# Optimization experiments

Measured on AMD Instinct MI355X. Metric: run time of the kernel, lower is better.

## Reference

```python
import jax, jax.numpy as jnp
import numpy as np

T = 512           # num_timestamps
D = 512           # video_embed_dim
V = 2048          # fmri_dim (voxels)
H = 128           # hidden_dim


def setup_inputs() -> dict:
    key = jax.random.key(0)
    k = jax.random.split(key, 8)
    s1 = 1.0 / np.sqrt(D)
    s2 = 1.0 / np.sqrt(H)
    return {
        "video_embeddings": jax.random.normal(k[0], (T, D), dtype=jnp.float32),
        # stacked per-voxel weights (torch Linear: y = x @ W.T + b; we store W already transposed as [in, out])
        "W1": jax.random.uniform(k[1], (V, D, H), jnp.float32, -s1, s1),
        "b1": jax.random.uniform(k[2], (V, H), jnp.float32, -s1, s1),
        "W2": jax.random.uniform(k[3], (V, H, H), jnp.float32, -s2, s2),
        "b2": jax.random.uniform(k[4], (V, H), jnp.float32, -s2, s2),
        "W3": jax.random.uniform(k[5], (V, H), jnp.float32, -s2, s2),
        "b3": jax.random.uniform(k[6], (V,), jnp.float32, -s2, s2),
    }


def reference(video_embeddings, W1, b1, W2, b2, W3, b3):
    # Per-voxel MLP expressed as batched GEMMs over the voxel axis.
    # Dropout is identity in eval mode.
    h = jax.nn.relu(jnp.einsum("td,vdh->tvh", video_embeddings, W1) + b1)  # [T,V,H]
    h = jax.nn.relu(jnp.einsum("tvh,vhg->tvg", h, W2) + b2)                 # [T,V,H]
    out = jnp.einsum("tvh,vh->tv", h, W3) + b3                               # [T,V]
    return out
```

## Files before the change

kernel.cpp:

```cpp
#include <hip/hip_runtime.h>
#include <hip/hip_bf16.h>

#define TT 512
#define DD 512
#define VV 2048
#define HH 128

typedef __attribute__((ext_vector_type(8))) short bf16x8;
typedef __attribute__((ext_vector_type(8))) unsigned short ushort8;
typedef __attribute__((ext_vector_type(4))) unsigned short ushort4v;
typedef __attribute__((ext_vector_type(4))) float f32x4;

__device__ __forceinline__ unsigned short f2bf(float f) {
  union { __hip_bfloat16 b; unsigned short u; } cv;
  cv.b = __float2bfloat16(f);
  return cv.u;
}

__device__ __forceinline__ void lds_barrier() {
  asm volatile("s_waitcnt lgkmcnt(0)\n\ts_barrier" ::: "memory");
}

#define VM_GATE(N)                                                   \
  do {                                                               \
    asm volatile("s_waitcnt vmcnt(" #N ")" ::: "memory");            \
    __builtin_amdgcn_sched_barrier(0);                               \
  } while (0)

__global__ void cvt_x_kernel(const float* __restrict__ x, unsigned short* __restrict__ xb) {
  const int i = blockIdx.x * blockDim.x + threadIdx.x;
  const float4 f = ((const float4*)x)[i];
  ushort4v u;
  u[0] = f2bf(f.x); u[1] = f2bf(f.y); u[2] = f2bf(f.z); u[3] = f2bf(f.w);
  ((ushort4v*)xb)[i] = u;
}

__global__ __launch_bounds__(512, 2)
void voxel_mlp_kernel(const unsigned short* __restrict__ Xb,
                      const float* __restrict__ W1,
                      const float* __restrict__ b1,
                      const float* __restrict__ W2,
                      const float* __restrict__ b2,
                      const float* __restrict__ W3,
                      const float* __restrict__ b3,
                      float* __restrict__ out) {
  __shared__ __align__(16) char LDS[98304];
  constexpr unsigned GBASE  = 0;
  constexpr unsigned FBASE  = 65536;
  constexpr unsigned W2BASE = 0;
  constexpr unsigned H1BASE = 32768;

  const int v   = blockIdx.x;
  const int tid = threadIdx.x;
  const int w   = tid >> 6;
  const int l   = tid & 63;
  const int lg  = l >> 4;
  const int ll  = l & 15;

  const float* W1v = W1 + (size_t)v * DD * HH;
  const float* W2v = W2 + (size_t)v * HH * HH;

  const size_t gsrc_lane = (size_t)((w * 8 + (l >> 5)) * HH + (l & 31) * 4);

#define G_ISSUE(t)                                                         \
  { const float* gp = W1v + (size_t)(t) * 64 * HH + gsrc_lane;             \
    const unsigned ldst = GBASE + (unsigned)((t) & 1) * 32768u +           \
                          (unsigned)w * 4096u;                             \
    _Pragma("unroll") for (int p = 0; p < 4; ++p)                          \
      __builtin_amdgcn_global_load_lds(                                    \
        (const __attribute__((address_space(1))) void*)(gp + p * 2 * HH),  \
        (__attribute__((address_space(3))) void*)(&LDS[ldst + p * 1024u]), \
        16, 0, 0); }

  G_ISSUE(0);
  G_ISSUE(1);

  f32x4 acc1[4][8];
#pragma unroll
  for (int mi = 0; mi < 4; ++mi)
#pragma unroll
    for (int n = 0; n < 8; ++n) acc1[mi][n] = f32x4{0.f, 0.f, 0.f, 0.f};

#pragma unroll
  for (int s = 0; s < 8; ++s) {
    VM_GATE(4);
    lds_barrier();

    bf16x8 aF[2][4];
#pragma unroll
    for (int ks = 0; ks < 2; ++ks)
#pragma unroll
      for (int mi = 0; mi < 4; ++mi)
        aF[ks][mi] = *(const bf16x8*)(Xb + (size_t)(w * 64 + mi * 16 + ll) * DD +
                                      s * 64 + ks * 32 + lg * 8);

    const unsigned gb = GBASE + (unsigned)(s & 1) * 32768u;
#pragma unroll
    for (int ks = 0; ks < 2; ++ks) {
      float t0[8];
#pragma unroll
      for (int j = 0; j < 8; ++j)
        t0[j] = *(const float*)(&LDS[gb + (unsigned)(((ks * 32 + lg * 8 + j) * HH) +
                                                     w * 16 + ll) * 4u]);
      ushort8 e;
#pragma unroll
      for (int j = 0; j < 8; ++j) e[j] = f2bf(t0[j]);
      *(ushort8*)(&LDS[FBASE + (unsigned)ks * 8192u + (unsigned)w * 1024u +
                       (unsigned)l * 16u]) = e;
    }

    lds_barrier();

    if (s < 6) G_ISSUE(s + 2);

#pragma unroll
    for (int ks = 0; ks < 2; ++ks)
#pragma unroll
      for (int n = 0; n < 8; ++n) {
        const bf16x8 b = *(const bf16x8*)(&LDS[FBASE + (unsigned)ks * 8192u +
                                               (unsigned)n * 1024u + (unsigned)l * 16u]);
#pragma unroll
        for (int mi = 0; mi < 4; ++mi)
          acc1[mi][n] = __builtin_amdgcn_mfma_f32_16x16x32_bf16(aF[ks][mi], b, acc1[mi][n], 0, 0, 0);
      }
  }
#undef G_ISSUE


  float b1v[8], b2v[8], w3v[8];
#pragma unroll
  for (int n = 0; n < 8; ++n) {
    b1v[n] = b1[v * HH + n * 16 + ll];
    b2v[n] = b2[v * HH + n * 16 + ll];
    w3v[n] = W3[v * HH + n * 16 + ll];
  }
  const float b3v = b3[v];

  {
    const int ki = w & 3, mb = (w >> 2) * 4;
    float w2t[4][8];
#pragma unroll
    for (int q = 0; q < 4; ++q)
#pragma unroll
      for (int j = 0; j < 8; ++j)
        w2t[q][j] = W2v[(ki * 32 + lg * 8 + j) * HH + (mb + q) * 16 + ll];
#pragma unroll
    for (int q = 0; q < 4; ++q) {
      ushort8 e;
#pragma unroll
      for (int j = 0; j < 8; ++j) e[j] = f2bf(w2t[q][j]);
      *(ushort8*)(&LDS[W2BASE + (unsigned)ki * 8192u + (unsigned)(mb + q) * 1024u +
                       (unsigned)l * 16u]) = e;
    }
  }
  lds_barrier();

  const unsigned slot = H1BASE + (unsigned)w * 4096u;

#pragma unroll
  for (int mi = 0; mi < 4; ++mi) {
#pragma unroll
    for (int n = 0; n < 8; ++n) {
#pragma unroll
      for (int r = 0; r < 4; ++r) {
        const int tl = lg * 4 + r;
        float hv = acc1[mi][n][r] + b1v[n];
        hv = fmaxf(hv, 0.f);
        const int h = n * 16 + ll;
        const unsigned byte = slot + (unsigned)tl * 256u +
                              (unsigned)((h * 2) ^ ((tl & 7) << 4));
        *(unsigned short*)(&LDS[byte]) = f2bf(hv);
      }
    }
    f32x4 acc2[8];
#pragma unroll
    for (int m = 0; m < 8; ++m) acc2[m] = f32x4{0.f, 0.f, 0.f, 0.f};
#pragma unroll
    for (int ki = 0; ki < 4; ++ki) {
      const int k0 = ki * 32 + lg * 8;
      const unsigned abyte = slot + (unsigned)ll * 256u +
                             (unsigned)((k0 * 2) ^ ((ll & 7) << 4));
      const bf16x8 a2 = *(const bf16x8*)(&LDS[abyte]);
#pragma unroll
      for (int m = 0; m < 8; ++m) {
        const bf16x8 bw = *(const bf16x8*)(&LDS[W2BASE + (unsigned)ki * 8192u +
                                                (unsigned)m * 1024u + (unsigned)l * 16u]);
        acc2[m] = __builtin_amdgcn_mfma_f32_16x16x32_bf16(a2, bw, acc2[m], 0, 0, 0);
      }
    }
#pragma unroll
    for (int r = 0; r < 4; ++r) {
      float p = 0.f;
#pragma unroll
      for (int m = 0; m < 8; ++m)
        p += fmaxf(acc2[m][r] + b2v[m], 0.f) * w3v[m];
      p += __shfl_xor(p, 1);
      p += __shfl_xor(p, 2);
      p += __shfl_xor(p, 4);
      p += __shfl_xor(p, 8);
      if (ll == 0) {
        const int t = w * 64 + mi * 16 + lg * 4 + r;
        out[t * VV + v] = p + b3v;
      }
    }
  }
}

extern "C" void kernel_launch(void* const* d_in, const int* in_sizes, int n_in,
                              void* d_out, int out_size, void* d_ws, size_t ws_size,
                              hipStream_t stream) {
  const float* X  = (const float*)d_in[0];
  const float* W1 = (const float*)d_in[1];
  const float* b1 = (const float*)d_in[2];
  const float* W2 = (const float*)d_in[3];
  const float* b2 = (const float*)d_in[4];
  const float* W3 = (const float*)d_in[5];
  const float* b3 = (const float*)d_in[6];
  float* out = (float*)d_out;

  unsigned short* Xb = (unsigned short*)d_ws;

  cvt_x_kernel<<<256, 256, 0, stream>>>(X, Xb);
  voxel_mlp_kernel<<<VV, 512, 0, stream>>>(Xb, W1, b1, W2, b2, W3, b3, out);
}
```

Measured before the change: 298.1 us.

## Split each voxel across two blocks by time, triple-buffer W1 with smaller LDS

Launches two blocks per voxel, each handling half the timestamps, with an XCD-aware mapping so both halves of a voxel land on the same XCD and can share W1 reads through L2. LDS shrinks to 64KB and launch bounds rise so more blocks fit per CU. The W1 pipeline moves to 32-row steps with a three-slot fp32 staging ring, a swizzled bf16 fragment layout and a single barrier per step. In exchange each voxel's W1/W2 weights are fetched and converted twice, which doubles conversion work and risks extra HBM traffic if the L2 sharing does not happen.

```diff
diff --git a/kernel.cpp b/kernel.cpp
--- a/kernel.cpp
+++ b/kernel.cpp
@@ -35,7 +35,7 @@
   ((ushort4v*)xb)[i] = u;
 }
 
-__global__ __launch_bounds__(512, 2)
+__global__ __launch_bounds__(512, 4)
 void voxel_mlp_kernel(const unsigned short* __restrict__ Xb,
                       const float* __restrict__ W1,
                       const float* __restrict__ b1,
@@ -44,13 +44,18 @@
                       const float* __restrict__ W3,
                       const float* __restrict__ b3,
                       float* __restrict__ out) {
-  __shared__ __align__(16) char LDS[98304];
+  __shared__ __align__(16) char LDS[65536];
   constexpr unsigned GBASE  = 0;
-  constexpr unsigned FBASE  = 65536;
+  constexpr unsigned FBASE  = 49152;
   constexpr unsigned W2BASE = 0;
   constexpr unsigned H1BASE = 32768;
 
-  const int v   = blockIdx.x;
+  const int bid  = blockIdx.x;
+  const int xcd  = bid & 7;
+  const int gg   = bid >> 3;
+  const int half = gg & 1;
+  const int v    = (gg >> 1) * 8 + xcd;
+
   const int tid = threadIdx.x;
   const int w   = tid >> 6;
   const int l   = tid & 63;
@@ -60,72 +65,77 @@
   const float* W1v = W1 + (size_t)v * DD * HH;
   const float* W2v = W2 + (size_t)v * HH * HH;
 
-  const size_t gsrc_lane = (size_t)((w * 8 + (l >> 5)) * HH + (l & 31) * 4);
-
-#define G_ISSUE(t)                                                         \
-  { const float* gp = W1v + (size_t)(t) * 64 * HH + gsrc_lane;             \
-    const unsigned ldst = GBASE + (unsigned)((t) & 1) * 32768u +           \
-                          (unsigned)w * 4096u;                             \
-    _Pragma("unroll") for (int p = 0; p < 4; ++p)                          \
-      __builtin_amdgcn_global_load_lds(                                    \
-        (const __attribute__((address_space(1))) void*)(gp + p * 2 * HH),  \
-        (__attribute__((address_space(3))) void*)(&LDS[ldst + p * 1024u]), \
+  const size_t gsrc = (size_t)((w * 4 + (l >> 5)) * HH + (l & 31) * 4);
+  const int n_c = l >> 3;
+  const int ll0 = (l & 7) * 2;
+
+#define G_ISSUE(t)                                                          \
+  { const float* gp = W1v + (size_t)(t) * 32 * HH + gsrc;                   \
+    const unsigned ldst = GBASE + (unsigned)((t) % 3) * 16384u +            \
+                          (unsigned)w * 2048u;                              \
+    _Pragma("unroll") for (int p = 0; p < 2; ++p)                           \
+      __builtin_amdgcn_global_load_lds(                                     \
+        (const __attribute__((address_space(1))) void*)(gp + p * 2 * HH),   \
+        (__attribute__((address_space(3))) void*)(&LDS[ldst + p * 1024u]),  \
         16, 0, 0); }
+
+#define CVT(tau)                                                            \
+  { const unsigned gs = GBASE + (unsigned)((tau) % 3) * 16384u;             \
+    ushort4v ev, ov;                                                        \
+    _Pragma("unroll") for (int r = 0; r < 4; ++r) {                         \
+      const float2 g2 = *(const float2*)(&LDS[gs +                          \
+          (unsigned)((w * 4 + r) * 512 + (n_c * 16 + ll0) * 4)]);           \
+      ev[r] = f2bf(g2.x); ov[r] = f2bf(g2.y); }                             \
+    const unsigned fb = FBASE + (unsigned)((tau) & 1) * 8192u +             \
+                        (unsigned)n_c * 1024u;                              \
+    const unsigned ca = (unsigned)((((w >> 1) * 16 + ll0) * 16) ^ (n_c << 4)); \
+    const unsigned cb = (unsigned)((((w >> 1) * 16 + ll0 + 1) * 16) ^ (n_c << 4)); \
+    *(ushort4v*)(&LDS[fb + ca + (unsigned)(w & 1) * 8u]) = ev;              \
+    *(ushort4v*)(&LDS[fb + cb + (unsigned)(w & 1) * 8u]) = ov; }
 
   G_ISSUE(0);
   G_ISSUE(1);
-
-  f32x4 acc1[4][8];
-#pragma unroll
-  for (int mi = 0; mi < 4; ++mi)
+  VM_GATE(2);
+  CVT(0);
+  lds_barrier();
+
+  f32x4 acc1[2][8];
+#pragma unroll
+  for (int mi = 0; mi < 2; ++mi)
 #pragma unroll
     for (int n = 0; n < 8; ++n) acc1[mi][n] = f32x4{0.f, 0.f, 0.f, 0.f};
 
 #pragma unroll
-  for (int s = 0; s < 8; ++s) {
-    VM_GATE(4);
+  for (int s = 0; s < 16; ++s) {
+    bf16x8 aF[2];
+#pragma unroll
+    for (int mi = 0; mi < 2; ++mi)
+      aF[mi] = *(const bf16x8*)(Xb + (size_t)(half * 256 + w * 32 + mi * 16 + ll) * DD +
+                                s * 32 + lg * 8);
+    __builtin_amdgcn_sched_barrier(0);
+
+    if (s < 14) {
+      G_ISSUE(s + 2);
+      VM_GATE(2);
+    } else if (s == 14) {
+      VM_GATE(0);
+    }
+
+    if (s < 15) CVT(s + 1);
+
+#pragma unroll
+    for (int n = 0; n < 8; ++n) {
+      const bf16x8 b = *(const bf16x8*)(&LDS[FBASE + (unsigned)(s & 1) * 8192u +
+                                             (unsigned)n * 1024u +
+                                             (unsigned)(((lg * 16 + ll) * 16) ^ (n << 4))]);
+#pragma unroll
+      for (int mi = 0; mi < 2; ++mi)
+        acc1[mi][n] = __builtin_amdgcn_mfma_f32_16x16x32_bf16(aF[mi], b, acc1[mi][n], 0, 0, 0);
+    }
     lds_barrier();
-
-    bf16x8 aF[2][4];
-#pragma unroll
-    for (int ks = 0; ks < 2; ++ks)
-#pragma unroll
-      for (int mi = 0; mi < 4; ++mi)
-        aF[ks][mi] = *(const bf16x8*)(Xb + (size_t)(w * 64 + mi * 16 + ll) * DD +
-                                      s * 64 + ks * 32 + lg * 8);
-
-    const unsigned gb = GBASE + (unsigned)(s & 1) * 32768u;
-#pragma unroll
-    for (int ks = 0; ks < 2; ++ks) {
-      float t0[8];
-#pragma unroll
-      for (int j = 0; j < 8; ++j)
-        t0[j] = *(const float*)(&LDS[gb + (unsigned)(((ks * 32 + lg * 8 + j) * HH) +
-                                                     w * 16 + ll) * 4u]);
-      ushort8 e;
-#pragma unroll
-      for (int j = 0; j < 8; ++j) e[j] = f2bf(t0[j]);
-      *(ushort8*)(&LDS[FBASE + (unsigned)ks * 8192u + (unsigned)w * 1024u +
-                       (unsigned)l * 16u]) = e;
-    }
-
-    lds_barrier();
-
-    if (s < 6) G_ISSUE(s + 2);
-
-#pragma unroll
-    for (int ks = 0; ks < 2; ++ks)
-#pragma unroll
-      for (int n = 0; n < 8; ++n) {
-        const bf16x8 b = *(const bf16x8*)(&LDS[FBASE + (unsigned)ks * 8192u +
-                                               (unsigned)n * 1024u + (unsigned)l * 16u]);
-#pragma unroll
-        for (int mi = 0; mi < 4; ++mi)
-          acc1[mi][n] = __builtin_amdgcn_mfma_f32_16x16x32_bf16(aF[ks][mi], b, acc1[mi][n], 0, 0, 0);
-      }
   }
 #undef G_ISSUE
-
+#undef CVT
 
   float b1v[8], b2v[8], w3v[8];
 #pragma unroll
@@ -158,7 +168,7 @@
   const unsigned slot = H1BASE + (unsigned)w * 4096u;
 
 #pragma unroll
-  for (int mi = 0; mi < 4; ++mi) {
+  for (int mi = 0; mi < 2; ++mi) {
 #pragma unroll
     for (int n = 0; n < 8; ++n) {
 #pragma unroll
@@ -199,7 +209,7 @@
       p += __shfl_xor(p, 4);
       p += __shfl_xor(p, 8);
       if (ll == 0) {
-        const int t = w * 64 + mi * 16 + lg * 4 + r;
+        const int t = half * 256 + w * 32 + mi * 16 + lg * 4 + r;
         out[t * VV + v] = p + b3v;
       }
     }
@@ -221,5 +231,5 @@
   unsigned short* Xb = (unsigned short*)d_ws;
 
   cvt_x_kernel<<<256, 256, 0, stream>>>(X, Xb);
-  voxel_mlp_kernel<<<VV, 512, 0, stream>>>(Xb, W1, b1, W2, b2, W3, b3, out);
-}
+  voxel_mlp_kernel<<<VV * 2, 512, 0, stream>>>(Xb, W1, b1, W2, b2, W3, b3, out);
+}
```

New measurement: 343.5 us. +15.2%, slower.
